# Kernel tuning notes

Hardware: AMD Instinct MI355X
Metric: run time of the kernel (lower is better)

The kernel has to match this reference:

```python
import jax, jax.numpy as jnp
import numpy as np

BATCH, SEQ, D_MODEL, D_STATE = 4, 2048, 512, 64
LN_EPS = 1e-5

def setup_inputs() -> dict:
    key = jax.random.key(0)
    ks = jax.random.split(key, 8)
    x = jax.random.normal(ks[0], (BATCH, SEQ, D_MODEL), jnp.float32)
    log_A_real = jax.random.normal(ks[1], (D_MODEL, D_STATE), jnp.float32)
    A_imag = jax.random.normal(ks[2], (D_MODEL, D_STATE), jnp.float32)
    B_param = jax.random.normal(ks[3], (D_MODEL, D_STATE, 2), jnp.float32) * 0.01
    C_param = jax.random.normal(ks[4], (D_MODEL, D_STATE, 2), jnp.float32) * 0.01
    D_param = jnp.ones((D_MODEL,), jnp.float32)
    W_out = jax.random.normal(ks[5], (D_MODEL, D_MODEL), jnp.float32) * (1.0 / np.sqrt(D_MODEL))
    b_out = jnp.zeros((D_MODEL,), jnp.float32)
    gamma = jnp.ones((D_MODEL,), jnp.float32)
    beta = jnp.zeros((D_MODEL,), jnp.float32)
    return dict(x=x, log_A_real=log_A_real, A_imag=A_imag, B_param=B_param,
                C_param=C_param, D_param=D_param, W_out=W_out, b_out=b_out,
                gamma=gamma, beta=beta)


def reference(x, log_A_real, A_imag, B_param, C_param, D_param, W_out, b_out, gamma, beta):
    Bn, L, d = x.shape
    # diagonal complex SSM parameters
    A = -jnp.exp(log_A_real) + 1j * A_imag                  # (d, s) complex, Re(A) < 0
    Bc = B_param[..., 0] + 1j * B_param[..., 1]              # (d, s)
    Cc = C_param[..., 0] + 1j * C_param[..., 1]              # (d, s)
    # kernel: K[d, l] = Re( sum_s conj(C) * exp(l*A) * B )
    powers = jnp.arange(L, dtype=jnp.float32)[:, None, None]  # (L,1,1)
    A_pow = jnp.exp(powers * A[None])                         # (L, d, s) complex
    CB = jnp.conj(Cc) * Bc                                    # (d, s)
    K = jnp.einsum('ds,lds->dl', CB, A_pow).real              # (d, L)
    # FFT convolution (matches torch flip + rfft conv + slice [L-1:2L-1])
    x_t = jnp.swapaxes(x, 1, 2)                               # (B, d, L)
    K_fl = jnp.flip(K, axis=-1)
    n = 2 * L
    Xf = jnp.fft.rfft(x_t, n=n, axis=-1)
    Kf = jnp.fft.rfft(K_fl, n=n, axis=-1)
    y = jnp.fft.irfft(Xf * Kf[None], n=n, axis=-1)[..., L - 1:2 * L - 1]
    y = y + D_param[None, :, None] * x_t                      # skip term D*x
    y = jnp.swapaxes(y, 1, 2)                                 # (B, L, d)
    y = y @ W_out.T + b_out                                   # out_proj (dropout p=0)
    z = y + x                                                 # residual
    mu = jnp.mean(z, axis=-1, keepdims=True)
    var = jnp.var(z, axis=-1, keepdims=True)
    return gamma * (z - mu) / jnp.sqrt(var + LN_EPS) + beta
```

## Files before the change

### kernel.cpp

```cpp
#include <hip/hip_runtime.h>
#include <hip/hip_bf16.h>
#include <stdint.h>
#include <stddef.h>

#define BATCH 4
#define SEQ   2048
#define DM    512
#define NST   64
#define LN_EPS 1e-5f
#define NCH   32
#define KDIM  192

typedef __attribute__((ext_vector_type(8))) short short8;
typedef __attribute__((ext_vector_type(4))) float f32x4;

__device__ __forceinline__ ushort f2bf(float f) {
    __hip_bfloat16 h = __float2bfloat16(f);
    return *(ushort*)&h;
}
__device__ __forceinline__ float bf2f(ushort u) {
    __hip_bfloat16 h = *(__hip_bfloat16*)&u;
    return __bfloat162float(h);
}

__global__ __launch_bounds__(256) void k_prep(
    const float* __restrict__ x, const float* __restrict__ W,
    __hip_bfloat16* __restrict__ xT, __hip_bfloat16* __restrict__ Wbf)
{
    __shared__ float smem[64][33];
    const int tid = threadIdx.x;
    const int bid = blockIdx.x;

    if (bid < 2048) {
        const int dt = bid & 15, lt = (bid >> 4) & 31, b = bid >> 9;
        const int l0 = lt * 64, d0 = dt * 32;
        const int dd = tid & 31, lr = tid >> 5;
        #pragma unroll
        for (int it = 0; it < 8; ++it) {
            int ll = it * 8 + lr;
            smem[ll][dd] = x[((size_t)b * SEQ + l0 + ll) * DM + d0 + dd];
        }
        __syncthreads();
        const int dw = tid >> 3, lg = (tid & 7) * 8;
        ushort pk[8];
        #pragma unroll
        for (int i = 0; i < 8; ++i) pk[i] = f2bf(smem[lg + i][dw]);
        *(short8*)&xT[((size_t)(d0 + dw) * BATCH + b) * SEQ + l0 + lg] = *(short8*)pk;
    } else {
        int i = (bid - 2048) * 256 + tid;
        if (i < DM * DM) Wbf[i] = __float2bfloat16(W[i]);
    }
}

__global__ __launch_bounds__(256) void k_ssm(
    const float* __restrict__ logA, const float* __restrict__ Aim,
    const float* __restrict__ Bp, const float* __restrict__ Cp,
    const __hip_bfloat16* __restrict__ xT, const float* __restrict__ Dp,
    __hip_bfloat16* __restrict__ yT)
{
    __shared__ short Zs[128 * 24 * 8];
    __shared__ __align__(16) char Rgn[128 * 129 * 4];
    __shared__ float Klds[64];
    __shared__ float2 e64s[64];
    short* Gs = (short*)Rgn;
    float (*Us)[129] = (float(*)[129])Rgn;
    short* Ms = (short*)Rgn;

    const int tid = threadIdx.x;
    const int d = blockIdx.x;
    const int w = tid >> 6, lane = tid & 63;
    const int q = lane >> 4, n = lane & 15;

    short8 xr[4];
    #pragma unroll
    for (int it = 0; it < 4; ++it) {
        int id = it * 256 + tid;
        int col = id >> 3, ck = id & 7;
        int bb = col >> 5, ch = col & 31;
        xr[it] = *(const short8*)&xT[((size_t)d * BATCH + bb) * SEQ + ch * 64 + ck * 8];
    }

    uint mca[16];
    {
        const int s = lane;
        const int i = d * NST + s;
        float aa  = expf(logA[i]);
        float wim = Aim[i];
        float mag = expf(-aa);
        float er = mag * cosf(wim), ei = mag * sinf(wim);
        float Br = Bp[2*i], Bi = Bp[2*i+1];
        float Cr = Cp[2*i], Ci = Cp[2*i+1];
        float CBr = Cr*Br + Ci*Bi;
        float CBi = Cr*Bi - Ci*Br;

        float t2r = er*er - ei*ei,     t2i = 2.f*er*ei;
        float t4r = t2r*t2r - t2i*t2i, t4i = 2.f*t2r*t2i;
        float t8r = t4r*t4r - t4i*t4i, t8i = 2.f*t4r*t4i;
        float g16r = t8r*t8r - t8i*t8i, g16i = 2.f*t8r*t8i;
        float ar, ai;
        if (w == 0)      { ar = 1.f;  ai = 0.f; }
        else if (w == 1) { ar = g16r; ai = g16i; }
        else {
            float g32r = g16r*g16r - g16i*g16i, g32i = 2.f*g16r*g16i;
            if (w == 2)  { ar = g32r; ai = g32i; }
            else         { ar = g32r*g16r - g32i*g16i; ai = g32r*g16i + g32i*g16r; }
        }
        float prr = CBr*ar - CBi*ai;
        float pii = CBr*ai + CBi*ar;

        float kb[16];
        ushort gR[16], gI[16];
        #pragma unroll
        for (int tt = 0; tt < 16; ++tt) {
            kb[tt] = prr;
            gR[tt] = f2bf(prr);
            gI[tt] = f2bf(pii);
            float npr = er*prr - ei*pii, npi = er*pii + ei*prr;  prr = npr; pii = npi;
            float nar = er*ar - ei*ai,   nai = er*ai + ei*ar;    ar = nar; ai = nai;
            mca[tt] = (uint)f2bf(ar) | ((uint)f2bf(-ai) << 16);
        }
        if (w == 3) e64s[s] = make_float2(ar, ai);

        short8 v;
        int row = 2 * s;
        #pragma unroll
        for (int e = 0; e < 8; ++e) v[e] = (short)gR[e];
        { int cs = (2*w) ^ (row & 7);     *(short8*)&Gs[(row * 8 + cs) * 8] = v; }
        #pragma unroll
        for (int e = 0; e < 8; ++e) v[e] = (short)gR[8 + e];
        { int cs = (2*w + 1) ^ (row & 7); *(short8*)&Gs[(row * 8 + cs) * 8] = v; }
        row = 2 * s + 1;
        #pragma unroll
        for (int e = 0; e < 8; ++e) v[e] = (short)gI[e];
        { int cs = (2*w) ^ (row & 7);     *(short8*)&Gs[(row * 8 + cs) * 8] = v; }
        #pragma unroll
        for (int e = 0; e < 8; ++e) v[e] = (short)gI[8 + e];
        { int cs = (2*w + 1) ^ (row & 7); *(short8*)&Gs[(row * 8 + cs) * 8] = v; }

        #pragma unroll
        for (int tt = 0; tt < 16; ++tt) {
            float v2 = kb[tt];
            #pragma unroll
            for (int mask = 1; mask < 64; mask <<= 1) v2 += __shfl_xor(v2, mask);
            if (lane == 0) Klds[16 * w + tt] = v2;
        }
    }

    #pragma unroll
    for (int it = 0; it < 4; ++it) {
        int id = it * 256 + tid;
        int col = id >> 3, ck = id & 7;
        int cs = ck ^ (col & 7);
        *(short8*)&Zs[(col * 24 + cs) * 8] = xr[it];
    }
    __syncthreads();

    f32x4 acc1[2][8];
    {
        #pragma unroll
        for (int rt = 0; rt < 2; ++rt)
            #pragma unroll
            for (int nf = 0; nf < 8; ++nf)
                #pragma unroll
                for (int k = 0; k < 4; ++k) acc1[rt][nf][k] = 0.f;

        #pragma unroll
        for (int rt = 0; rt < 2; ++rt) {
            const int arow = w * 32 + rt * 16 + n;
            #pragma unroll
            for (int kt = 0; kt < 2; ++kt) {
                int c = kt * 4 + q;
                int csa = c ^ (arow & 7);
                short8 af = *(const short8*)&Gs[(arow * 8 + csa) * 8];
                #pragma unroll
                for (int nf = 0; nf < 8; ++nf) {
                    int col = nf * 16 + n;
                    int csb = c ^ (col & 7);
                    short8 bf = *(const short8*)&Zs[(col * 24 + csb) * 8];
                    acc1[rt][nf] = __builtin_amdgcn_mfma_f32_16x16x32_bf16(af, bf, acc1[rt][nf], 0, 0, 0);
                }
            }
        }
    }
    __syncthreads();

    #pragma unroll
    for (int rt = 0; rt < 2; ++rt) {
        const int r0w = w * 32 + rt * 16 + q * 4;
        #pragma unroll
        for (int nf = 0; nf < 8; ++nf) {
            int col = nf * 16 + n;
            #pragma unroll
            for (int r = 0; r < 4; ++r) Us[r0w + r][col] = acc1[rt][nf][r];
        }
    }
    __syncthreads();

    {
        const int bb = tid >> 6, s = tid & 63;
        const int st = s >> 2, so = (s & 3) * 2;
        float2 a64 = e64s[s];
        const float er = a64.x, ei = a64.y;
        {
            int col = bb * 32 + 31;
            int c = 8 + st, cs = (c & ~7) | ((c & 7) ^ (col & 7));
            *(uint*)&Zs[(col * 24 + cs) * 8 + so] = 0u;
        }
        float gr = Us[2 * s][bb * 32 + 31], gi = Us[2 * s + 1][bb * 32 + 31];
        {
            int col = bb * 32 + 30;
            int c = 8 + st, cs = (c & ~7) | ((c & 7) ^ (col & 7));
            *(uint*)&Zs[(col * 24 + cs) * 8 + so] = (uint)f2bf(gr) | ((uint)f2bf(gi) << 16);
        }
        for (int ch = 30; ch >= 1; --ch) {
            float ur = Us[2 * s][bb * 32 + ch], ui = Us[2 * s + 1][bb * 32 + ch];
            float nr = ur + er * gr - ei * gi;
            float ni = ui + er * gi + ei * gr;
            gr = nr; gi = ni;
            int col = bb * 32 + ch - 1;
            int c = 8 + st, cs = (c & ~7) | ((c & 7) ^ (col & 7));
            *(uint*)&Zs[(col * 24 + cs) * 8 + so] = (uint)f2bf(gr) | ((uint)f2bf(gi) << 16);
        }
    }
    __syncthreads();

    {
        #pragma unroll
        for (int it = 0; it < 2; ++it) {
            int id = it * 256 + tid;
            int row = id >> 3, c = id & 7;
            short8 v;
            #pragma unroll
            for (int e = 0; e < 8; ++e) {
                int col = c * 8 + e;
                float kv = (col >= row) ? Klds[col - row] : 0.f;
                v[e] = (short)f2bf(kv);
            }
            int cs = c ^ (row & 7);
            *(short8*)&Ms[(row * 24 + cs) * 8] = v;
        }
        const int s = lane;
        const int cc = 8 + (s >> 2);
        const int soff = 2 * (s & 3);
        #pragma unroll
        for (int tt = 0; tt < 16; ++tt) {
            int row = 63 - (16 * w + tt);
            int cs = (cc & ~7) | ((cc & 7) ^ (row & 7));
            *(uint*)&Ms[(row * 24 + cs) * 8 + soff] = mca[tt];
        }
    }
    __syncthreads();

    f32x4 acc[8];
    #pragma unroll
    for (int nf = 0; nf < 8; ++nf)
        #pragma unroll
        for (int k = 0; k < 4; ++k) acc[nf][k] = 0.f;

    const int arow = w * 16 + n;
    #pragma unroll
    for (int kt = 0; kt < 6; ++kt) {
        int c = kt * 4 + q;
        int csa = (c & ~7) | ((c & 7) ^ (arow & 7));
        short8 af = *(const short8*)&Ms[(arow * 24 + csa) * 8];
        #pragma unroll
        for (int nf = 0; nf < 8; ++nf) {
            int col = nf * 16 + n;
            int csb = (c & ~7) | ((c & 7) ^ (col & 7));
            short8 bfr = *(const short8*)&Zs[(col * 24 + csb) * 8];
            acc[nf] = __builtin_amdgcn_mfma_f32_16x16x32_bf16(af, bfr, acc[nf], 0, 0, 0);
        }
    }

    const float Dd = Dp[d];
    const int i0 = w * 16 + q * 4;
    #pragma unroll
    for (int nf = 0; nf < 8; ++nf) {
        int col = nf * 16 + n;
        int bb = col >> 5, ch = col & 31;
        int cx = (i0 >> 3) ^ (col & 7);
        const ushort* zp = (const ushort*)&Zs[(col * 24 + cx) * 8 + (i0 & 7)];
        ushort o[4];
        #pragma unroll
        for (int r = 0; r < 4; ++r)
            o[r] = f2bf(acc[nf][r] + Dd * bf2f(zp[r]));
        *(uint2*)&yT[((size_t)d * BATCH + bb) * SEQ + ch * 64 + i0] = *(uint2*)o;
    }
}

__global__ __launch_bounds__(512) void k_gemm_ln(
    const __hip_bfloat16* __restrict__ yT, const __hip_bfloat16* __restrict__ Wbf,
    const float* __restrict__ x, const float* __restrict__ bout,
    const float* __restrict__ gamma, const float* __restrict__ beta,
    float* __restrict__ out)
{
    __shared__ short Af[32][520];
    __shared__ short Bs[512][32];
    __shared__ float red[8][32][2];
    __shared__ float stats[32][2];

    const int tid  = threadIdx.x;
    const int w    = tid >> 6;
    const int lane = tid & 63;
    const int q    = lane >> 4;
    const int m    = lane & 15;
    const int r0   = blockIdx.x * 32;
    const int bq   = r0 >> 11;
    const int l0   = r0 & 2047;

    {
        const int kdb = tid >> 3, lg = (tid & 7) * 4;
        uint2 u[8];
        #pragma unroll
        for (int j = 0; j < 8; ++j)
            u[j] = *(const uint2*)&yT[((size_t)(j * 64 + kdb) * BATCH + bq) * SEQ + l0 + lg];
        #pragma unroll
        for (int j = 0; j < 8; ++j) {
            int kd = j * 64 + kdb;
            Af[lg + 0][kd] = (short)(u[j].x & 0xffff);
            Af[lg + 1][kd] = (short)(u[j].x >> 16);
            Af[lg + 2][kd] = (short)(u[j].y & 0xffff);
            Af[lg + 3][kd] = (short)(u[j].y >> 16);
        }
    }

    short8 nb0, nb1, nb2, nb3;
    const int ob = tid >> 2, jb = tid & 3;
    const int js = (jb ^ (ob & 3)) * 8;
    #define LOADB(k0) { \
        nb0 = *(const short8*)(Wbf + (size_t)(ob      ) * DM + (k0) + jb * 8); \
        nb1 = *(const short8*)(Wbf + (size_t)(ob + 128) * DM + (k0) + jb * 8); \
        nb2 = *(const short8*)(Wbf + (size_t)(ob + 256) * DM + (k0) + jb * 8); \
        nb3 = *(const short8*)(Wbf + (size_t)(ob + 384) * DM + (k0) + jb * 8); }
    #define WRITEB() { \
        *(short8*)&Bs[ob      ][js] = nb0; \
        *(short8*)&Bs[ob + 128][js] = nb1; \
        *(short8*)&Bs[ob + 256][js] = nb2; \
        *(short8*)&Bs[ob + 384][js] = nb3; }

    LOADB(0);
    WRITEB();
    LOADB(32);
    __syncthreads();

    f32x4 acc[2][4];
    #pragma unroll
    for (int a = 0; a < 2; ++a)
        #pragma unroll
        for (int nn = 0; nn < 4; ++nn)
            #pragma unroll
            for (int k = 0; k < 4; ++k) acc[a][nn][k] = 0.f;

    for (int k = 0; k < 16; ++k) {
        const int k0 = k * 32;
        short8 a0 = *(const short8*)&Af[m][k0 + q * 8];
        short8 a1 = *(const short8*)&Af[16 + m][k0 + q * 8];
        #pragma unroll
        for (int nf = 0; nf < 4; ++nf) {
            int o = w * 64 + nf * 16 + m;
            short8 bb = *(const short8*)&Bs[o][(q ^ (m & 3)) * 8];
            acc[0][nf] = __builtin_amdgcn_mfma_f32_16x16x32_bf16(a0, bb, acc[0][nf], 0, 0, 0);
            acc[1][nf] = __builtin_amdgcn_mfma_f32_16x16x32_bf16(a1, bb, acc[1][nf], 0, 0, 0);
        }
        __syncthreads();
        if (k < 15) {
            WRITEB();
            if (k < 14) LOADB((k + 2) * 32);
            __syncthreads();
        }
    }
    #undef LOADB
    #undef WRITEB

    float bo[4], ga[4], be[4];
    #pragma unroll
    for (int nf = 0; nf < 4; ++nf) {
        int o = w * 64 + nf * 16 + m;
        bo[nf] = bout[o]; ga[nf] = gamma[o]; be[nf] = beta[o];
    }

    float rs[2][4], rq[2][4];
    #pragma unroll
    for (int mf = 0; mf < 2; ++mf)
        #pragma unroll
        for (int i = 0; i < 4; ++i) { rs[mf][i] = 0.f; rq[mf][i] = 0.f; }

    #pragma unroll
    for (int mf = 0; mf < 2; ++mf)
        #pragma unroll
        for (int nf = 0; nf < 4; ++nf) {
            int o = w * 64 + nf * 16 + m;
            #pragma unroll
            for (int i = 0; i < 4; ++i) {
                int row = mf * 16 + q * 4 + i;
                float zv = acc[mf][nf][i] + bo[nf] + x[(size_t)(r0 + row) * DM + o];
                acc[mf][nf][i] = zv;
                rs[mf][i] += zv;
                rq[mf][i] += zv * zv;
            }
        }

    #pragma unroll
    for (int mask = 1; mask < 16; mask <<= 1) {
        #pragma unroll
        for (int mf = 0; mf < 2; ++mf)
            #pragma unroll
            for (int i = 0; i < 4; ++i) {
                rs[mf][i] += __shfl_xor(rs[mf][i], mask);
                rq[mf][i] += __shfl_xor(rq[mf][i], mask);
            }
    }
    if (m == 0) {
        #pragma unroll
        for (int mf = 0; mf < 2; ++mf)
            #pragma unroll
            for (int i = 0; i < 4; ++i) {
                int row = mf * 16 + q * 4 + i;
                red[w][row][0] = rs[mf][i];
                red[w][row][1] = rq[mf][i];
            }
    }
    __syncthreads();
    if (tid < 32) {
        float s = 0.f, sq = 0.f;
        #pragma unroll
        for (int ww = 0; ww < 8; ++ww) { s += red[ww][tid][0]; sq += red[ww][tid][1]; }
        float mu  = s * (1.f / DM);
        float var = sq * (1.f / DM) - mu * mu;
        stats[tid][0] = mu;
        stats[tid][1] = 1.f / sqrtf(var + LN_EPS);
    }
    __syncthreads();

    #pragma unroll
    for (int mf = 0; mf < 2; ++mf)
        #pragma unroll
        for (int i = 0; i < 4; ++i) {
            int row = mf * 16 + q * 4 + i;
            float mu = stats[row][0], rstd = stats[row][1];
            #pragma unroll
            for (int nf = 0; nf < 4; ++nf) {
                int o = w * 64 + nf * 16 + m;
                out[(size_t)(r0 + row) * DM + o] =
                    ga[nf] * (acc[mf][nf][i] - mu) * rstd + be[nf];
            }
        }
}

extern "C" void kernel_launch(void* const* d_in, const int* in_sizes, int n_in,
                              void* d_out, int out_size, void* d_ws, size_t ws_size,
                              hipStream_t stream)
{
    const float* x    = (const float*)d_in[0];
    const float* logA = (const float*)d_in[1];
    const float* Aim  = (const float*)d_in[2];
    const float* Bp   = (const float*)d_in[3];
    const float* Cp   = (const float*)d_in[4];
    const float* Dp   = (const float*)d_in[5];
    const float* W    = (const float*)d_in[6];
    const float* bo   = (const float*)d_in[7];
    const float* ga   = (const float*)d_in[8];
    const float* be   = (const float*)d_in[9];

    char* ws = (char*)d_ws;
    __hip_bfloat16* Wbf = (__hip_bfloat16*)ws;
    __hip_bfloat16* xT  = (__hip_bfloat16*)(ws + (3u << 20));
    __hip_bfloat16* yT  = (__hip_bfloat16*)(ws + (41u << 20));

    k_prep   <<<3072, 256, 0, stream>>>(x, W, xT, Wbf);
    k_ssm    <<<DM, 256, 0, stream>>>(logA, Aim, Bp, Cp, xT, Dp, yT);
    k_gemm_ln<<<(BATCH * SEQ) / 32, 512, 0, stream>>>(yT, Wbf, x, bo, ga, be, (float*)d_out);
}
```

Baseline: 52.57 us.

## Run SSM kernel with 8 waves per block, halving per-wave work

Doubles the k_ssm block to 512 threads. Work is split so each wave computes 8 kernel taps instead of 16, one 16-row MFMA tile in the chunk-state GEMM, and half the column tiles in the output GEMM. The serial inter-chunk scan still runs on only the first 256 threads, now with partial unrolling. The aim is more latency hiding and shorter per-wave critical paths, at the cost of more register/LDS pressure per block and idle waves during the scan.

```diff
diff --git a/kernel.cpp b/kernel.cpp
--- a/kernel.cpp
+++ b/kernel.cpp
@@ -52,7 +52,7 @@
     }
 }
 
-__global__ __launch_bounds__(256) void k_ssm(
+__global__ __launch_bounds__(512) void k_ssm(
     const float* __restrict__ logA, const float* __restrict__ Aim,
     const float* __restrict__ Bp, const float* __restrict__ Cp,
     const __hip_bfloat16* __restrict__ xT, const float* __restrict__ Dp,
@@ -71,16 +71,16 @@
     const int w = tid >> 6, lane = tid & 63;
     const int q = lane >> 4, n = lane & 15;
 
-    short8 xr[4];
-    #pragma unroll
-    for (int it = 0; it < 4; ++it) {
-        int id = it * 256 + tid;
+    short8 xr[2];
+    #pragma unroll
+    for (int it = 0; it < 2; ++it) {
+        int id = it * 512 + tid;
         int col = id >> 3, ck = id & 7;
         int bb = col >> 5, ch = col & 31;
         xr[it] = *(const short8*)&xT[((size_t)d * BATCH + bb) * SEQ + ch * 64 + ck * 8];
     }
 
-    uint mca[16];
+    uint mca[8];
     {
         const int s = lane;
         const int i = d * NST + s;
@@ -93,25 +93,34 @@
         float CBr = Cr*Br + Ci*Bi;
         float CBi = Cr*Bi - Ci*Br;
 
-        float t2r = er*er - ei*ei,     t2i = 2.f*er*ei;
-        float t4r = t2r*t2r - t2i*t2i, t4i = 2.f*t2r*t2i;
-        float t8r = t4r*t4r - t4i*t4i, t8i = 2.f*t4r*t4i;
-        float g16r = t8r*t8r - t8i*t8i, g16i = 2.f*t8r*t8i;
+        float e2r = er*er - ei*ei,   e2i = 2.f*er*ei;
+        float e4r = e2r*e2r - e2i*e2i, e4i = 2.f*e2r*e2i;
+        float e8r = e4r*e4r - e4i*e4i, e8i = 2.f*e4r*e4i;
         float ar, ai;
         if (w == 0)      { ar = 1.f;  ai = 0.f; }
-        else if (w == 1) { ar = g16r; ai = g16i; }
+        else if (w == 1) { ar = e8r;  ai = e8i; }
         else {
-            float g32r = g16r*g16r - g16i*g16i, g32i = 2.f*g16r*g16i;
-            if (w == 2)  { ar = g32r; ai = g32i; }
-            else         { ar = g32r*g16r - g32i*g16i; ai = g32r*g16i + g32i*g16r; }
+            float e16r = e8r*e8r - e8i*e8i, e16i = 2.f*e8r*e8i;
+            if (w == 2)      { ar = e16r; ai = e16i; }
+            else if (w == 3) { ar = e16r*e8r - e16i*e8i;  ai = e16r*e8i + e16i*e8r; }
+            else {
+                float e32r = e16r*e16r - e16i*e16i, e32i = 2.f*e16r*e16i;
+                if (w == 4)      { ar = e32r; ai = e32i; }
+                else if (w == 5) { ar = e32r*e8r - e32i*e8i;   ai = e32r*e8i + e32i*e8r; }
+                else if (w == 6) { ar = e32r*e16r - e32i*e16i; ai = e32r*e16i + e32i*e16r; }
+                else {
+                    float e48r = e32r*e16r - e32i*e16i, e48i = e32r*e16i + e32i*e16r;
+                    ar = e48r*e8r - e48i*e8i;  ai = e48r*e8i + e48i*e8r;
+                }
+            }
         }
         float prr = CBr*ar - CBi*ai;
         float pii = CBr*ai + CBi*ar;
 
-        float kb[16];
-        ushort gR[16], gI[16];
-        #pragma unroll
-        for (int tt = 0; tt < 16; ++tt) {
+        float kb[8];
+        ushort gR[8], gI[8];
+        #pragma unroll
+        for (int tt = 0; tt < 8; ++tt) {
             kb[tt] = prr;
             gR[tt] = f2bf(prr);
             gI[tt] = f2bf(pii);
@@ -119,84 +128,72 @@
             float nar = er*ar - ei*ai,   nai = er*ai + ei*ar;    ar = nar; ai = nai;
             mca[tt] = (uint)f2bf(ar) | ((uint)f2bf(-ai) << 16);
         }
-        if (w == 3) e64s[s] = make_float2(ar, ai);
+        if (w == 7) e64s[s] = make_float2(ar, ai);
 
         short8 v;
         int row = 2 * s;
         #pragma unroll
         for (int e = 0; e < 8; ++e) v[e] = (short)gR[e];
-        { int cs = (2*w) ^ (row & 7);     *(short8*)&Gs[(row * 8 + cs) * 8] = v; }
-        #pragma unroll
-        for (int e = 0; e < 8; ++e) v[e] = (short)gR[8 + e];
-        { int cs = (2*w + 1) ^ (row & 7); *(short8*)&Gs[(row * 8 + cs) * 8] = v; }
+        { int cs = w ^ (row & 7); *(short8*)&Gs[(row * 8 + cs) * 8] = v; }
         row = 2 * s + 1;
         #pragma unroll
         for (int e = 0; e < 8; ++e) v[e] = (short)gI[e];
-        { int cs = (2*w) ^ (row & 7);     *(short8*)&Gs[(row * 8 + cs) * 8] = v; }
-        #pragma unroll
-        for (int e = 0; e < 8; ++e) v[e] = (short)gI[8 + e];
-        { int cs = (2*w + 1) ^ (row & 7); *(short8*)&Gs[(row * 8 + cs) * 8] = v; }
-
-        #pragma unroll
-        for (int tt = 0; tt < 16; ++tt) {
+        { int cs = w ^ (row & 7); *(short8*)&Gs[(row * 8 + cs) * 8] = v; }
+
+        #pragma unroll
+        for (int tt = 0; tt < 8; ++tt) {
             float v2 = kb[tt];
             #pragma unroll
             for (int mask = 1; mask < 64; mask <<= 1) v2 += __shfl_xor(v2, mask);
-            if (lane == 0) Klds[16 * w + tt] = v2;
-        }
-    }
-
-    #pragma unroll
-    for (int it = 0; it < 4; ++it) {
-        int id = it * 256 + tid;
+            if (lane == 0) Klds[8 * w + tt] = v2;
+        }
+    }
+
+    #pragma unroll
+    for (int it = 0; it < 2; ++it) {
+        int id = it * 512 + tid;
         int col = id >> 3, ck = id & 7;
         int cs = ck ^ (col & 7);
         *(short8*)&Zs[(col * 24 + cs) * 8] = xr[it];
     }
     __syncthreads();
 
-    f32x4 acc1[2][8];
+    f32x4 acc1[8];
     {
         #pragma unroll
-        for (int rt = 0; rt < 2; ++rt)
-            #pragma unroll
-            for (int nf = 0; nf < 8; ++nf)
-                #pragma unroll
-                for (int k = 0; k < 4; ++k) acc1[rt][nf][k] = 0.f;
-
-        #pragma unroll
-        for (int rt = 0; rt < 2; ++rt) {
-            const int arow = w * 32 + rt * 16 + n;
-            #pragma unroll
-            for (int kt = 0; kt < 2; ++kt) {
-                int c = kt * 4 + q;
-                int csa = c ^ (arow & 7);
-                short8 af = *(const short8*)&Gs[(arow * 8 + csa) * 8];
-                #pragma unroll
-                for (int nf = 0; nf < 8; ++nf) {
-                    int col = nf * 16 + n;
-                    int csb = c ^ (col & 7);
-                    short8 bf = *(const short8*)&Zs[(col * 24 + csb) * 8];
-                    acc1[rt][nf] = __builtin_amdgcn_mfma_f32_16x16x32_bf16(af, bf, acc1[rt][nf], 0, 0, 0);
-                }
-            }
-        }
-    }
-    __syncthreads();
-
-    #pragma unroll
-    for (int rt = 0; rt < 2; ++rt) {
-        const int r0w = w * 32 + rt * 16 + q * 4;
+        for (int nf = 0; nf < 8; ++nf)
+            #pragma unroll
+            for (int k = 0; k < 4; ++k) acc1[nf][k] = 0.f;
+
+        const int arow = w * 16 + n;
+        #pragma unroll
+        for (int kt = 0; kt < 2; ++kt) {
+            int c = kt * 4 + q;
+            int csa = c ^ (arow & 7);
+            short8 af = *(const short8*)&Gs[(arow * 8 + csa) * 8];
+            #pragma unroll
+            for (int nf = 0; nf < 8; ++nf) {
+                int col = nf * 16 + n;
+                int csb = c ^ (col & 7);
+                short8 bf = *(const short8*)&Zs[(col * 24 + csb) * 8];
+                acc1[nf] = __builtin_amdgcn_mfma_f32_16x16x32_bf16(af, bf, acc1[nf], 0, 0, 0);
+            }
+        }
+    }
+    __syncthreads();
+
+    {
+        const int r0w = w * 16 + q * 4;
         #pragma unroll
         for (int nf = 0; nf < 8; ++nf) {
             int col = nf * 16 + n;
             #pragma unroll
-            for (int r = 0; r < 4; ++r) Us[r0w + r][col] = acc1[rt][nf][r];
-        }
-    }
-    __syncthreads();
-
-    {
+            for (int r = 0; r < 4; ++r) Us[r0w + r][col] = acc1[nf][r];
+        }
+    }
+    __syncthreads();
+
+    if (tid < 256) {
         const int bb = tid >> 6, s = tid & 63;
         const int st = s >> 2, so = (s & 3) * 2;
         float2 a64 = e64s[s];
@@ -212,6 +209,7 @@
             int c = 8 + st, cs = (c & ~7) | ((c & 7) ^ (col & 7));
             *(uint*)&Zs[(col * 24 + cs) * 8 + so] = (uint)f2bf(gr) | ((uint)f2bf(gi) << 16);
         }
+        #pragma unroll 6
         for (int ch = 30; ch >= 1; --ch) {
             float ur = Us[2 * s][bb * 32 + ch], ui = Us[2 * s + 1][bb * 32 + ch];
             float nr = ur + er * gr - ei * gi;
@@ -225,9 +223,8 @@
     __syncthreads();
 
     {
-        #pragma unroll
-        for (int it = 0; it < 2; ++it) {
-            int id = it * 256 + tid;
+        {
+            int id = tid;
             int row = id >> 3, c = id & 7;
             short8 v;
             #pragma unroll
@@ -243,47 +240,48 @@
         const int cc = 8 + (s >> 2);
         const int soff = 2 * (s & 3);
         #pragma unroll
-        for (int tt = 0; tt < 16; ++tt) {
-            int row = 63 - (16 * w + tt);
+        for (int tt = 0; tt < 8; ++tt) {
+            int row = 63 - (8 * w + tt);
             int cs = (cc & ~7) | ((cc & 7) ^ (row & 7));
             *(uint*)&Ms[(row * 24 + cs) * 8 + soff] = mca[tt];
         }
     }
     __syncthreads();
 
-    f32x4 acc[8];
-    #pragma unroll
-    for (int nf = 0; nf < 8; ++nf)
+    f32x4 acc[4];
+    #pragma unroll
+    for (int nf = 0; nf < 4; ++nf)
         #pragma unroll
         for (int k = 0; k < 4; ++k) acc[nf][k] = 0.f;
 
-    const int arow = w * 16 + n;
+    const int arow = (w >> 1) * 16 + n;
+    const int nfb  = (w & 1) * 4;
     #pragma unroll
     for (int kt = 0; kt < 6; ++kt) {
         int c = kt * 4 + q;
         int csa = (c & ~7) | ((c & 7) ^ (arow & 7));
         short8 af = *(const short8*)&Ms[(arow * 24 + csa) * 8];
         #pragma unroll
-        for (int nf = 0; nf < 8; ++nf) {
-            int col = nf * 16 + n;
+        for (int j = 0; j < 4; ++j) {
+            int col = (nfb + j) * 16 + n;
             int csb = (c & ~7) | ((c & 7) ^ (col & 7));
             short8 bfr = *(const short8*)&Zs[(col * 24 + csb) * 8];
-            acc[nf] = __builtin_amdgcn_mfma_f32_16x16x32_bf16(af, bfr, acc[nf], 0, 0, 0);
+            acc[j] = __builtin_amdgcn_mfma_f32_16x16x32_bf16(af, bfr, acc[j], 0, 0, 0);
         }
     }
 
     const float Dd = Dp[d];
-    const int i0 = w * 16 + q * 4;
-    #pragma unroll
-    for (int nf = 0; nf < 8; ++nf) {
-        int col = nf * 16 + n;
+    const int i0 = (w >> 1) * 16 + q * 4;
+    #pragma unroll
+    for (int j = 0; j < 4; ++j) {
+        int col = (nfb + j) * 16 + n;
         int bb = col >> 5, ch = col & 31;
         int cx = (i0 >> 3) ^ (col & 7);
         const ushort* zp = (const ushort*)&Zs[(col * 24 + cx) * 8 + (i0 & 7)];
         ushort o[4];
         #pragma unroll
         for (int r = 0; r < 4; ++r)
-            o[r] = f2bf(acc[nf][r] + Dd * bf2f(zp[r]));
+            o[r] = f2bf(acc[j][r] + Dd * bf2f(zp[r]));
         *(uint2*)&yT[((size_t)d * BATCH + bb) * SEQ + ch * 64 + i0] = *(uint2*)o;
     }
 }
@@ -468,6 +466,6 @@
     __hip_bfloat16* yT  = (__hip_bfloat16*)(ws + (41u << 20));
 
     k_prep   <<<3072, 256, 0, stream>>>(x, W, xT, Wbf);
-    k_ssm    <<<DM, 256, 0, stream>>>(logA, Aim, Bp, Cp, xT, Dp, yT);
+    k_ssm    <<<DM, 512, 0, stream>>>(logA, Aim, Bp, Cp, xT, Dp, yT);
     k_gemm_ln<<<(BATCH * SEQ) / 32, 512, 0, stream>>>(yT, Wbf, x, bo, ga, be, (float*)d_out);
 }
```

Result: faster. 48.50 us (-7.7%).
